# Performance work log

Hardware: AMD Instinct MI355X
Metric: run time of the kernel (lower is better)

The kernel has to match this reference:

```python
import jax, jax.numpy as jnp
import numpy as np
from jax import lax

N, M, K, D = 2048, 64, 32, 512
C = 1.0


def setup_inputs() -> dict:
    key = jax.random.key(0)
    k1, k2, k3, k4 = jax.random.split(key, 4)
    W = jax.random.normal(k1, (K, D), dtype=jnp.float32) * 0.05
    T = jax.random.normal(k2, (K, K), dtype=jnp.float32) * 0.05
    data = jax.random.normal(k3, (N, M, D), dtype=jnp.float32)
    labels = jax.random.randint(k4, (N, M), 0, K, dtype=jnp.int32)
    return {"W": W, "T": T, "data": data, "labels": labels}


def _crf_word(W, T, data, labels):
    # data: [m, d], labels: [m] int. dots: [m, K] emission scores.
    dots = data @ W.T
    m = dots.shape[0]
    k = T.shape[0]

    # alpha[i, k] = logsumexp_j(dots[i-1, j] + alpha[i-1, j] + T[j, k]); alpha[0] = 0
    def alpha_step(prev, d_prev):
        a = jax.nn.logsumexp(prev[:, None] + d_prev[:, None] + T, axis=0)
        return a, a
    _, alphas = lax.scan(alpha_step, jnp.zeros((k,), dots.dtype), dots[:-1])
    alpha = jnp.concatenate([jnp.zeros((1, k), dots.dtype), alphas], axis=0)  # [m, K]

    # beta[i, k] = logsumexp_j(dots[i+1, j] + beta[i+1, j] + T[k, j]); beta[m-1] = 0
    def beta_step(prev, d_next):
        b = jax.nn.logsumexp(prev[None, :] + d_next[None, :] + T, axis=1)
        return b, b
    _, betas = lax.scan(beta_step, jnp.zeros((k,), dots.dtype), dots[1:][::-1])
    beta = jnp.concatenate([betas[::-1], jnp.zeros((1, k), dots.dtype)], axis=0)  # [m, K]

    # unary marginals p1 [m, K]
    p1 = jax.nn.softmax(alpha + beta + dots, axis=-1)
    # pairwise marginals p2 [m-1, K, K]; softmax over flattened KxK per position
    s = (alpha[:-1] + dots[:-1])[:, :, None] + (beta[1:] + dots[1:])[:, None, :] + T[None, :, :]
    p2 = jax.nn.softmax(s.reshape(m - 1, k * k), axis=-1).reshape(m - 1, k, k)

    # log P(y|x)
    logZ = jax.nn.logsumexp(dots[-1] + alpha[-1])
    emit = jnp.take_along_axis(dots, labels[:, None], axis=1).sum()
    trans = T[labels[:-1], labels[1:]].sum()
    logpyx = emit + trans - logZ

    # analytic gradients (as computed by the module, not autodiff)
    onehot = jax.nn.one_hot(labels, k, dtype=dots.dtype)          # [m, K]
    dw = (onehot - p1).T @ data                                    # [K, d]
    trans_oh = onehot[:-1][:, :, None] * onehot[1:][:, None, :]    # [m-1, K, K]
    dT = (trans_oh - p2).sum(axis=0)                               # [K, K]
    return logpyx, dw, dT


def reference(W, T, data, labels):
    logpyx, dw, dT = jax.vmap(_crf_word, in_axes=(None, None, 0, 0))(W, T, data, labels)
    meandw = dw.mean(axis=0)
    meandT = dT.mean(axis=0)
    gradients = jnp.concatenate([meandw.ravel(), meandT.ravel()])
    # objValue (stored on the module) -- computed for faithfulness though forward returns gradients
    obj = -C * logpyx.mean() + 0.5 * jnp.sum(W ** 2) + 0.5 * jnp.sum(T ** 2)
    del obj
    return gradients
```

## Files before the change

kernel.cpp:

```cpp
#include <hip/hip_runtime.h>
#include <math.h>

typedef __bf16 bf16x8 __attribute__((ext_vector_type(8)));
typedef float f32x4 __attribute__((ext_vector_type(4)));

__device__ __forceinline__ bf16x8 to_bf16x8(float4 a, float4 b) {
    bf16x8 r;
    r[0] = (__bf16)a.x; r[1] = (__bf16)a.y; r[2] = (__bf16)a.z; r[3] = (__bf16)a.w;
    r[4] = (__bf16)b.x; r[5] = (__bf16)b.y; r[6] = (__bf16)b.z; r[7] = (__bf16)b.w;
    return r;
}
#define MFMA16(A, B, C) __builtin_amdgcn_mfma_f32_16x16x32_bf16((A), (B), (C), 0, 0, 0)

__device__ __forceinline__ float rsum32(float v) {
    v += __shfl_xor(v, 1, 32); v += __shfl_xor(v, 2, 32);
    v += __shfl_xor(v, 4, 32); v += __shfl_xor(v, 8, 32);
    v += __shfl_xor(v, 16, 32);
    return v;
}

__device__ __forceinline__ float rl(float v, int j) {
    return __int_as_float(__builtin_amdgcn_readlane(__float_as_int(v), j));
}
#define RL_MATVEC(T, EV, OUT)                                                  \
    {                                                                          \
        float a0_ = 0.f, a1_ = 0.f, a2_ = 0.f, a3_ = 0.f;                      \
        _Pragma("unroll") for (int j_ = 0; j_ < 32; j_ += 4) {                 \
            a0_ += EV[j_ + 0] * rl((T), j_ + 0);                               \
            a1_ += EV[j_ + 1] * rl((T), j_ + 1);                               \
            a2_ += EV[j_ + 2] * rl((T), j_ + 2);                               \
            a3_ += EV[j_ + 3] * rl((T), j_ + 3);                               \
        }                                                                      \
        OUT = (a0_ + a1_) + (a2_ + a3_);                                       \
    }

__global__ __launch_bounds__(256) void k_prep(const float* __restrict__ W,
                                              bf16x8* __restrict__ wsW) {
    const int e = blockIdx.x * 256 + threadIdx.x;
    const int gk = e >> 7, h = (e >> 6) & 1, l = e & 63;
    const float* src = W + (size_t)(h * 16 + (l & 15)) * 512 + gk * 32 + (l >> 4) * 8;
    float4 lo = *(const float4*)src, hi = *(const float4*)(src + 4);
    wsW[e] = to_bf16x8(lo, hi);
}

__global__ __launch_bounds__(128) void k_word(const float* __restrict__ data,
                                              const bf16x8* __restrict__ wsW,
                                              const float* __restrict__ Tm,
                                              const int* __restrict__ labels,
                                              float* __restrict__ Pdiff,
                                              float* __restrict__ dTpart) {
    __shared__ __align__(16) __bf16 gdb[2048];
    __shared__ __align__(16) __bf16 Unb[2048];
    __shared__ __align__(16) __bf16 Mb[2048];
    __shared__ float Sb[1024];
    __shared__ float bscale[64];
    __shared__ int lab[64];

    const int n = blockIdx.x;
    const int tid = threadIdx.x;
    const int wv = tid >> 6;
    const int lane = tid & 63;
    const int k = tid & 31;
    const int hw = tid >> 5;
    float* drow = Pdiff + (size_t)n * 2048;

    {
        const int m16 = lane & 15;
        const int kb = lane >> 4;
        const size_t row0 = (size_t)n * 64 + wv * 32;
        const float* arow0 = data + (row0 + m16) * 512 + kb * 8;
        const float* arow1 = arow0 + 16 * 512;

        f32x4 acc00 = {0.f, 0.f, 0.f, 0.f}, acc01 = {0.f, 0.f, 0.f, 0.f};
        f32x4 acc10 = {0.f, 0.f, 0.f, 0.f}, acc11 = {0.f, 0.f, 0.f, 0.f};

#pragma unroll 2
        for (int kk = 0; kk < 16; ++kk) {
            const int off = kk * 32;
            float4 a0l = *(const float4*)(arow0 + off);
            float4 a0h = *(const float4*)(arow0 + off + 4);
            float4 a1l = *(const float4*)(arow1 + off);
            float4 a1h = *(const float4*)(arow1 + off + 4);
            bf16x8 a0 = to_bf16x8(a0l, a0h), a1 = to_bf16x8(a1l, a1h);
            bf16x8 b0 = wsW[kk * 128 + lane];
            bf16x8 b1 = wsW[kk * 128 + 64 + lane];
            acc00 = MFMA16(a0, b0, acc00);
            acc01 = MFMA16(a0, b1, acc01);
            acc10 = MFMA16(a1, b0, acc10);
            acc11 = MFMA16(a1, b1, acc11);
        }
        const int ib = wv * 32 + kb * 4;
#pragma unroll
        for (int r = 0; r < 4; ++r) {
            gdb[(ib + r) * 32 + m16]           = (__bf16)__expf(acc00[r]);
            gdb[(ib + r) * 32 + 16 + m16]      = (__bf16)__expf(acc01[r]);
            gdb[(ib + 16 + r) * 32 + m16]      = (__bf16)__expf(acc10[r]);
            gdb[(ib + 16 + r) * 32 + 16 + m16] = (__bf16)__expf(acc11[r]);
        }
    }
#pragma unroll
    for (int i = 0; i < 8; ++i) Sb[tid * 8 + i] = 0.f;
    if (tid < 64) { lab[tid] = labels[n * 64 + tid]; bscale[tid] = 1.f; }
    __syncthreads();

    if (wv == 0) {
        float Ecol[32];
#pragma unroll
        for (int j = 0; j < 32; ++j) Ecol[j] = __expf(Tm[j * 32 + k]);
        float Areg = 1.f;
        float gdc = (float)gdb[k];
#pragma unroll 1
        for (int g = 0; g < 16; ++g) {
#pragma unroll
            for (int ii = 0; ii < 4; ++ii) {
                const int i = g * 4 + ii;
                float t = Areg * gdc;
                Unb[i * 32 + k] = (__bf16)t;
                if (i < 63) {
                    gdc = (float)gdb[(i + 1) * 32 + k];
                    float anew;
                    RL_MATVEC(t, Ecol, anew);
                    Areg = anew;
                }
            }
            if (g < 15) Areg *= __builtin_amdgcn_rcpf(rsum32(Areg));
        }
    } else {
        float Erow[32];
#pragma unroll
        for (int j = 0; j < 32; ++j) Erow[j] = __expf(Tm[k * 32 + j]);
        float Mreg = 1.f;
        Mb[63 * 32 + k] = (__bf16)1.f;
        float gdc = (float)gdb[63 * 32 + k];
#pragma unroll 1
        for (int g = 0; g < 16; ++g) {
#pragma unroll
            for (int ii = 0; ii < 4; ++ii) {
                const int s = g * 4 + ii;
                if (s < 63) {
                    const int i = 63 - s;
                    float ww = gdc * Mreg;
                    gdc = (float)gdb[(i - 1) * 32 + k];
                    float m2;
                    RL_MATVEC(ww, Erow, m2);
                    Mb[(i - 1) * 32 + k] = (__bf16)m2;
                    Mreg = m2;
                }
            }
            if (g < 15) {
                float rc = __builtin_amdgcn_rcpf(rsum32(Mreg));
                Mreg *= rc;
                if (lane == 0) bscale[58 - 4 * g] = rc;
            }
        }
    }
    __syncthreads();

    float Scol[32];
#pragma unroll
    for (int j = 0; j < 32; ++j) Scol[j] = 0.f;
    const int i0 = hw * 16;
    for (int ii = 0; ii < 16; ++ii) {
        const int i = i0 + ii;
        float un = (float)Unb[i * 32 + k];
        float mm = (float)Mb[i * 32 + k];
        float t = un * mm;
        float Z = rsum32(t);
        float rZ = __builtin_amdgcn_rcpf(Z);
        float pd = ((lab[i] == k) ? 1.f : 0.f) - t * rZ;
        drow[i * 32 + k] = pd;
        if (i < 63) {
            float f = (float)gdb[(i + 1) * 32 + k] * (float)Mb[(i + 1) * 32 + k]
                      * rZ * bscale[i];
            const bf16x8* uv = (const bf16x8*)(&Unb[i * 32]);
            bf16x8 u0 = uv[0], u1 = uv[1], u2 = uv[2], u3 = uv[3];
#pragma unroll
            for (int j = 0; j < 8; ++j) Scol[j]      += (float)u0[j] * f;
#pragma unroll
            for (int j = 0; j < 8; ++j) Scol[8 + j]  += (float)u1[j] * f;
#pragma unroll
            for (int j = 0; j < 8; ++j) Scol[16 + j] += (float)u2[j] * f;
#pragma unroll
            for (int j = 0; j < 8; ++j) Scol[24 + j] += (float)u3[j] * f;
        }
    }
#pragma unroll
    for (int j = 0; j < 32; ++j) atomicAdd(&Sb[j * 32 + k], Scol[j]);
    __syncthreads();

    float* op = dTpart + (size_t)n * 1024;
#pragma unroll
    for (int e = 0; e < 8; ++e) {
        const int idx = tid * 8 + e;
        op[idx] = -__expf(Tm[idx]) * Sb[idx];
    }
    __syncthreads();
    if (tid < 63) atomicAdd(&op[lab[tid] * 32 + lab[tid + 1]], 1.0f);
}

__global__ __launch_bounds__(256) void k_dw(const float* __restrict__ data,
                                            const float* __restrict__ Pd,
                                            float* __restrict__ dwp) {
    const int g = blockIdx.x >> 2;
    const int q = blockIdx.x & 3;
    const int tid = threadIdx.x;
    const int kg = __builtin_amdgcn_readfirstlane(tid >> 6);
    const int lane = tid & 63;
    const int k0 = kg << 3;
    const int d0 = q * 128 + lane * 2;

    float2 acc[8];
#pragma unroll
    for (int i = 0; i < 8; ++i) acc[i] = make_float2(0.f, 0.f);

    const size_t rbase = (size_t)g * 512;
    const float* dptr = data + rbase * 512 + d0;
    const float4* pptr = (const float4*)(Pd + rbase * 32) + kg * 2;

#define FMA8_2(PA, PB, DV)                                                     \
    acc[0].x += (PA).x * (DV).x; acc[0].y += (PA).x * (DV).y;                  \
    acc[1].x += (PA).y * (DV).x; acc[1].y += (PA).y * (DV).y;                  \
    acc[2].x += (PA).z * (DV).x; acc[2].y += (PA).z * (DV).y;                  \
    acc[3].x += (PA).w * (DV).x; acc[3].y += (PA).w * (DV).y;                  \
    acc[4].x += (PB).x * (DV).x; acc[4].y += (PB).x * (DV).y;                  \
    acc[5].x += (PB).y * (DV).x; acc[5].y += (PB).y * (DV).y;                  \
    acc[6].x += (PB).z * (DV).x; acc[6].y += (PB).z * (DV).y;                  \
    acc[7].x += (PB).w * (DV).x; acc[7].y += (PB).w * (DV).y;

    for (int r = 0; r < 512; r += 4) {
        float2 dv0 = *(const float2*)(dptr + (size_t)(r + 0) * 512);
        float2 dv1 = *(const float2*)(dptr + (size_t)(r + 1) * 512);
        float2 dv2 = *(const float2*)(dptr + (size_t)(r + 2) * 512);
        float2 dv3 = *(const float2*)(dptr + (size_t)(r + 3) * 512);
        float4 pa0 = pptr[(r + 0) * 8], pb0 = pptr[(r + 0) * 8 + 1];
        float4 pa1 = pptr[(r + 1) * 8], pb1 = pptr[(r + 1) * 8 + 1];
        float4 pa2 = pptr[(r + 2) * 8], pb2 = pptr[(r + 2) * 8 + 1];
        float4 pa3 = pptr[(r + 3) * 8], pb3 = pptr[(r + 3) * 8 + 1];
        FMA8_2(pa0, pb0, dv0)
        FMA8_2(pa1, pb1, dv1)
        FMA8_2(pa2, pb2, dv2)
        FMA8_2(pa3, pb3, dv3)
    }
#undef FMA8_2

    float* op = dwp + (size_t)g * 16384;
#pragma unroll
    for (int kk = 0; kk < 8; ++kk)
        *(float2*)(op + (k0 + kk) * 512 + d0) = acc[kk];
}

__global__ __launch_bounds__(256) void k_final(const float* __restrict__ dwp,
                                               const float* __restrict__ dTp,
                                               float* __restrict__ out) {
    __shared__ float red[256];
    const int b = blockIdx.x, t = threadIdx.x;
    const float inv = 1.0f / 2048.0f;
    if (b < 256) {
        const int q = t >> 6, ol = t & 63;
        const int oi = b * 64 + ol;
        float s = 0.f;
#pragma unroll 4
        for (int j = 0; j < 64; ++j) s += dwp[(size_t)(q * 64 + j) * 16384 + oi];
        red[t] = s;
        __syncthreads();
        if (t < 64) out[b * 64 + t] = (red[t] + red[t + 64] + red[t + 128] + red[t + 192]) * inv;
    } else {
        const int ol = t >> 4, q = t & 15;
        const int oi = (b - 256) * 16 + ol;
        float s = 0.f;
#pragma unroll 4
        for (int j = 0; j < 128; ++j) s += dTp[(size_t)(q * 128 + j) * 1024 + oi];
        s += __shfl_xor(s, 1, 16); s += __shfl_xor(s, 2, 16);
        s += __shfl_xor(s, 4, 16); s += __shfl_xor(s, 8, 16);
        if (q == 0) out[16384 + oi] = s * inv;
    }
}

extern "C" void kernel_launch(void* const* d_in, const int* in_sizes, int n_in,
                              void* d_out, int out_size, void* d_ws, size_t ws_size,
                              hipStream_t stream) {
    const float* W = (const float*)d_in[0];
    const float* Tm = (const float*)d_in[1];
    const float* data = (const float*)d_in[2];
    const int* labels = (const int*)d_in[3];
    float* out = (float*)d_out;
    float* ws = (float*)d_ws;

    float* Pdiff = ws;
    float* dTpart = ws + 4194304;
    float* dwpart = ws + 6291456;
    bf16x8* wsW = (bf16x8*)(ws + 10485760);

    hipLaunchKernelGGL(k_prep, dim3(8), dim3(256), 0, stream, W, wsW);
    hipLaunchKernelGGL(k_word, dim3(2048), dim3(128), 0, stream,
                       data, wsW, Tm, labels, Pdiff, dTpart);
    hipLaunchKernelGGL(k_dw, dim3(1024), dim3(256), 0, stream, data, Pdiff, dwpart);
    hipLaunchKernelGGL(k_final, dim3(320), dim3(256), 0, stream, dwpart, dTpart, out);
}
```

Baseline: 230.0 us.

## Widen k_word to 256 threads, splitting GEMM and marginal work across four waves

```diff
diff --git a/kernel.cpp b/kernel.cpp
--- a/kernel.cpp
+++ b/kernel.cpp
@@ -43,12 +43,12 @@
     wsW[e] = to_bf16x8(lo, hi);
 }
 
-__global__ __launch_bounds__(128) void k_word(const float* __restrict__ data,
-                                              const bf16x8* __restrict__ wsW,
-                                              const float* __restrict__ Tm,
-                                              const int* __restrict__ labels,
-                                              float* __restrict__ Pdiff,
-                                              float* __restrict__ dTpart) {
+__global__ __launch_bounds__(256, 6) void k_word(const float* __restrict__ data,
+                                                 const bf16x8* __restrict__ wsW,
+                                                 const float* __restrict__ Tm,
+                                                 const int* __restrict__ labels,
+                                                 float* __restrict__ Pdiff,
+                                                 float* __restrict__ dTpart) {
     __shared__ __align__(16) __bf16 gdb[2048];
     __shared__ __align__(16) __bf16 Unb[2048];
     __shared__ __align__(16) __bf16 Mb[2048];
@@ -67,39 +67,31 @@
     {
         const int m16 = lane & 15;
         const int kb = lane >> 4;
-        const size_t row0 = (size_t)n * 64 + wv * 32;
-        const float* arow0 = data + (row0 + m16) * 512 + kb * 8;
-        const float* arow1 = arow0 + 16 * 512;
-
-        f32x4 acc00 = {0.f, 0.f, 0.f, 0.f}, acc01 = {0.f, 0.f, 0.f, 0.f};
-        f32x4 acc10 = {0.f, 0.f, 0.f, 0.f}, acc11 = {0.f, 0.f, 0.f, 0.f};
+        const size_t row0 = (size_t)n * 64 + wv * 16;
+        const float* arow = data + (row0 + m16) * 512 + kb * 8;
+
+        f32x4 acc0 = {0.f, 0.f, 0.f, 0.f}, acc1 = {0.f, 0.f, 0.f, 0.f};
 
 #pragma unroll 2
         for (int kk = 0; kk < 16; ++kk) {
             const int off = kk * 32;
-            float4 a0l = *(const float4*)(arow0 + off);
-            float4 a0h = *(const float4*)(arow0 + off + 4);
-            float4 a1l = *(const float4*)(arow1 + off);
-            float4 a1h = *(const float4*)(arow1 + off + 4);
-            bf16x8 a0 = to_bf16x8(a0l, a0h), a1 = to_bf16x8(a1l, a1h);
+            float4 al = *(const float4*)(arow + off);
+            float4 ah = *(const float4*)(arow + off + 4);
+            bf16x8 a = to_bf16x8(al, ah);
             bf16x8 b0 = wsW[kk * 128 + lane];
             bf16x8 b1 = wsW[kk * 128 + 64 + lane];
-            acc00 = MFMA16(a0, b0, acc00);
-            acc01 = MFMA16(a0, b1, acc01);
-            acc10 = MFMA16(a1, b0, acc10);
-            acc11 = MFMA16(a1, b1, acc11);
-        }
-        const int ib = wv * 32 + kb * 4;
+            acc0 = MFMA16(a, b0, acc0);
+            acc1 = MFMA16(a, b1, acc1);
+        }
+        const int ib = wv * 16 + kb * 4;
 #pragma unroll
         for (int r = 0; r < 4; ++r) {
-            gdb[(ib + r) * 32 + m16]           = (__bf16)__expf(acc00[r]);
-            gdb[(ib + r) * 32 + 16 + m16]      = (__bf16)__expf(acc01[r]);
-            gdb[(ib + 16 + r) * 32 + m16]      = (__bf16)__expf(acc10[r]);
-            gdb[(ib + 16 + r) * 32 + 16 + m16] = (__bf16)__expf(acc11[r]);
-        }
-    }
-#pragma unroll
-    for (int i = 0; i < 8; ++i) Sb[tid * 8 + i] = 0.f;
+            gdb[(ib + r) * 32 + m16]      = (__bf16)__expf(acc0[r]);
+            gdb[(ib + r) * 32 + 16 + m16] = (__bf16)__expf(acc1[r]);
+        }
+    }
+#pragma unroll
+    for (int i = 0; i < 4; ++i) Sb[tid * 4 + i] = 0.f;
     if (tid < 64) { lab[tid] = labels[n * 64 + tid]; bscale[tid] = 1.f; }
     __syncthreads();
 
@@ -125,7 +117,7 @@
             }
             if (g < 15) Areg *= __builtin_amdgcn_rcpf(rsum32(Areg));
         }
-    } else {
+    } else if (wv == 1) {
         float Erow[32];
 #pragma unroll
         for (int j = 0; j < 32; ++j) Erow[j] = __expf(Tm[k * 32 + j]);
@@ -159,8 +151,8 @@
     float Scol[32];
 #pragma unroll
     for (int j = 0; j < 32; ++j) Scol[j] = 0.f;
-    const int i0 = hw * 16;
-    for (int ii = 0; ii < 16; ++ii) {
+    const int i0 = hw * 8;
+    for (int ii = 0; ii < 8; ++ii) {
         const int i = i0 + ii;
         float un = (float)Unb[i * 32 + k];
         float mm = (float)Mb[i * 32 + k];
@@ -190,8 +182,8 @@
 
     float* op = dTpart + (size_t)n * 1024;
 #pragma unroll
-    for (int e = 0; e < 8; ++e) {
-        const int idx = tid * 8 + e;
+    for (int e = 0; e < 4; ++e) {
+        const int idx = tid * 4 + e;
         op[idx] = -__expf(Tm[idx]) * Sb[idx];
     }
     __syncthreads();
@@ -292,7 +284,7 @@
     bf16x8* wsW = (bf16x8*)(ws + 10485760);
 
     hipLaunchKernelGGL(k_prep, dim3(8), dim3(256), 0, stream, W, wsW);
-    hipLaunchKernelGGL(k_word, dim3(2048), dim3(128), 0, stream,
+    hipLaunchKernelGGL(k_word, dim3(2048), dim3(256), 0, stream,
                        data, wsW, Tm, labels, Pdiff, dTpart);
     hipLaunchKernelGGL(k_dw, dim3(1024), dim3(256), 0, stream, data, Pdiff, dwpart);
     hipLaunchKernelGGL(k_final, dim3(320), dim3(256), 0, stream, dwpart, dTpart, out);
```

Measured after the change: 269.3 us. 1.17x slower.
